# Performance work log

Measured on AMD Instinct MI355X. Metric: run time of the kernel, lower is better.

Reference implementation:

```python
import jax, jax.numpy as jnp
import numpy as np

EMBED_DIM = 1024
NUM_HEADS = 16
HEAD_DIM = EMBED_DIM // NUM_HEADS
FF_DIM = 4096
B, T = 4, 1024


def setup_inputs() -> dict:
    key = jax.random.key(0)
    ks = jax.random.split(key, 13)
    E, F = EMBED_DIM, FF_DIM
    s_e = 1.0 / np.sqrt(E)
    s_f = 1.0 / np.sqrt(F)
    return {
        "x": jax.random.normal(ks[0], (B, T, E), dtype=jnp.float32),
        "ln1_w": jnp.ones((E,), jnp.float32),
        "ln1_b": jnp.zeros((E,), jnp.float32),
        "ln2_w": jnp.ones((E,), jnp.float32),
        "ln2_b": jnp.zeros((E,), jnp.float32),
        "qkv_w": jax.random.uniform(ks[1], (3 * E, E), jnp.float32, -s_e, s_e),
        "qkv_b": jax.random.uniform(ks[2], (3 * E,), jnp.float32, -s_e, s_e),
        "out_w": jax.random.uniform(ks[3], (E, E), jnp.float32, -s_e, s_e),
        "out_b": jax.random.uniform(ks[4], (E,), jnp.float32, -s_e, s_e),
        "fc1_w": jax.random.uniform(ks[5], (F, E), jnp.float32, -s_e, s_e),
        "fc1_b": jax.random.uniform(ks[6], (F,), jnp.float32, -s_e, s_e),
        "fc2_w": jax.random.uniform(ks[7], (E, F), jnp.float32, -s_f, s_f),
        "fc2_b": jax.random.uniform(ks[8], (E,), jnp.float32, -s_f, s_f),
    }


def _layer_norm(x, w, b, eps=1e-5):
    mu = jnp.mean(x, axis=-1, keepdims=True)
    var = jnp.mean(jnp.square(x - mu), axis=-1, keepdims=True)
    return (x - mu) * jax.lax.rsqrt(var + eps) * w + b


def reference(x, ln1_w, ln1_b, ln2_w, ln2_b, qkv_w, qkv_b, out_w, out_b,
              fc1_w, fc1_b, fc2_w, fc2_b):
    Bn, Tn, C = x.shape
    H, D = NUM_HEADS, HEAD_DIM

    # --- causal self-attention (pre-LN) ---
    h = _layer_norm(x, ln1_w, ln1_b)
    qkv = h @ qkv_w.T + qkv_b  # [B,T,3E]
    qkv = qkv.reshape(Bn, Tn, 3, H, D).transpose(2, 0, 3, 1, 4)  # [3,B,H,T,D]
    q, k, v = qkv[0], qkv[1], qkv[2]
    scores = jnp.einsum("bhtd,bhsd->bhts", q, k) / np.sqrt(D).astype(np.float32)
    causal = jnp.tril(jnp.ones((Tn, Tn), dtype=bool))
    scores = jnp.where(causal, scores, -jnp.inf)
    probs = jax.nn.softmax(scores, axis=-1)  # dropout is identity at eval
    attn = jnp.einsum("bhts,bhsd->bhtd", probs, v)
    attn = attn.transpose(0, 2, 1, 3).reshape(Bn, Tn, C)
    attn = attn @ out_w.T + out_b
    x = x + attn

    # --- GELU MLP (pre-LN) ---
    h = _layer_norm(x, ln2_w, ln2_b)
    h = jax.nn.gelu(h @ fc1_w.T + fc1_b, approximate=False)
    h = h @ fc2_w.T + fc2_b
    return x + h
```

## Files before the change

### kernel.cpp

```cpp
#include <hip/hip_runtime.h>

typedef float floatx4 __attribute__((ext_vector_type(4)));
typedef short shortx8 __attribute__((ext_vector_type(8)));

#define E_DIM 1024
#define F_DIM 4096
#define BATCH 4
#define SEQ 1024
#define NH 16
#define HD 64
#define MROWS (BATCH*SEQ)
#define QKV_N (3*E_DIM)

typedef const __attribute__((address_space(1))) unsigned int* gas_ptr;
typedef __attribute__((address_space(3))) unsigned int* las_ptr;

__device__ __forceinline__ unsigned short f2bf(float f) {
    union { float f; unsigned u; } un; un.f = f;
    unsigned u = un.u;
    u += 0x7fffu + ((u >> 16) & 1u);
    return (unsigned short)(u >> 16);
}

__device__ __forceinline__ float gelu_fast(float v) {
    float u = 0.7978845608f * (v + 0.044715f * v * v * v);
    float t = __builtin_exp2f(-2.885390082f * u);
    return v * __builtin_amdgcn_rcpf(1.0f + t);
}

__device__ __forceinline__ void xcd_remap(int& m_idx, int& n_idx) {
    int nt = gridDim.x;
    int mt_x = gridDim.y >> 3;
    int lin = blockIdx.y * nt + blockIdx.x;
    int xcd = lin & 7, loc = lin >> 3;
    int n = loc / mt_x;
    int m_local = loc - n * mt_x;
    m_idx = xcd * mt_x + m_local;
    n_idx = n;
}

#define S_QKV (3*E_DIM*E_DIM)
#define S_WO  (E_DIM*E_DIM)
#define S_W1  (F_DIM*E_DIM)
#define S_TOT (S_QKV + S_WO + 2*S_W1)
__global__ __launch_bounds__(256) void f2b_all(
        const float* __restrict__ qkv_w, const float* __restrict__ out_w,
        const float* __restrict__ fc1_w, const float* __restrict__ fc2_w,
        unsigned short* __restrict__ wq, unsigned short* __restrict__ wo,
        unsigned short* __restrict__ w1, unsigned short* __restrict__ w2) {
    long idx = ((long)blockIdx.x * 256 + threadIdx.x) * 4;
    const float* src; unsigned short* dst; long off;
    if (idx < S_QKV)                    { src = qkv_w; dst = wq; off = idx; }
    else if (idx < S_QKV + S_WO)        { src = out_w; dst = wo; off = idx - S_QKV; }
    else if (idx < S_QKV + S_WO + S_W1) { src = fc1_w; dst = w1; off = idx - S_QKV - S_WO; }
    else                                { src = fc2_w; dst = w2; off = idx - S_QKV - S_WO - S_W1; }
    float4 v = *(const float4*)&src[off];
    ushort4 o;
    o.x = f2bf(v.x); o.y = f2bf(v.y); o.z = f2bf(v.z); o.w = f2bf(v.w);
    *(ushort4*)&dst[off] = o;
}

__global__ __launch_bounds__(256) void ln_kernel(const float* __restrict__ x,
                                                 const float* __restrict__ w,
                                                 const float* __restrict__ b,
                                                 unsigned short* __restrict__ out) {
    int row = blockIdx.x;
    const float* xr = x + (size_t)row * E_DIM;
    float v[4];
    float s = 0.f, ss = 0.f;
    for (int i = 0; i < 4; ++i) {
        v[i] = xr[threadIdx.x + i * 256];
        s += v[i]; ss += v[i] * v[i];
    }
    for (int m = 32; m; m >>= 1) { s += __shfl_xor(s, m); ss += __shfl_xor(ss, m); }
    __shared__ float red[8];
    int wave = threadIdx.x >> 6;
    if ((threadIdx.x & 63) == 0) { red[wave] = s; red[wave + 4] = ss; }
    __syncthreads();
    s = red[0] + red[1] + red[2] + red[3];
    ss = red[4] + red[5] + red[6] + red[7];
    float mu = s * (1.0f / E_DIM);
    float var = ss * (1.0f / E_DIM) - mu * mu;
    float rs = rsqrtf(var + 1e-5f);
    for (int i = 0; i < 4; ++i) {
        int c = threadIdx.x + i * 256;
        out[(size_t)row * E_DIM + c] = f2bf((v[i] - mu) * rs * w[c] + b[c]);
    }
}

#define TM 128
#define TN 128
#define BK 64

template<int EPI>
__global__ __launch_bounds__(256) void gemm_bt(
        const unsigned short* __restrict__ A, const unsigned short* __restrict__ Bw,
        const float* __restrict__ bias, const float* __restrict__ resid,
        float* __restrict__ Cf, unsigned short* __restrict__ Cb,
        int M, int N, int K) {
    __shared__ unsigned short sA[2][TM * BK];
    __shared__ unsigned short sB[2][TN * BK];
    int tid = threadIdx.x;
    int wave = tid >> 6, lane = tid & 63;
    int m_idx, n_idx;
    xcd_remap(m_idx, n_idx);
    int n0 = n_idx * TN, m0 = m_idx * TM;
    int wm = (wave & 1) * 64, wn = (wave >> 1) * 64;
    int l15 = lane & 15, quad = lane >> 4;

    int srow = wave * 32 + (lane >> 3);
    int scg  = (lane & 7) ^ (srow & 7);
    const unsigned short* Ag = A  + (size_t)(m0 + srow) * K + scg * 8;
    const unsigned short* Bg = Bw + (size_t)(n0 + srow) * K + scg * 8;

    floatx4 acc[4][4];
#pragma unroll
    for (int i = 0; i < 4; ++i)
#pragma unroll
        for (int j = 0; j < 4; ++j) acc[i][j] = (floatx4)0.f;

    auto stage = [&](int kt, int bsel) {
        int k0 = kt * BK;
#pragma unroll
        for (int p = 0; p < 4; ++p) {
            __builtin_amdgcn_global_load_lds((gas_ptr)(Ag + k0 + p * 8 * K),
                (las_ptr)&sA[bsel][(wave * 32 + p * 8) * BK], 16, 0, 0);
            __builtin_amdgcn_global_load_lds((gas_ptr)(Bg + k0 + p * 8 * K),
                (las_ptr)&sB[bsel][(wave * 32 + p * 8) * BK], 16, 0, 0);
        }
    };

    int T = K / BK;
    stage(0, 0);
    stage(1, 1);
    for (int i = 0; i < T; ++i) {
        if (i + 1 < T) { asm volatile("s_waitcnt vmcnt(8)" ::: "memory"); }
        else           { asm volatile("s_waitcnt vmcnt(0)" ::: "memory"); }
        __builtin_amdgcn_s_barrier();
        int bs = i & 1;
#pragma unroll
        for (int kk8 = 0; kk8 < 8; kk8 += 4) {
            shortx8 af[4], bfr[4];
#pragma unroll
            for (int ii = 0; ii < 4; ++ii) {
                int R = wm + ii * 16 + l15;
                int sc = (quad + kk8) ^ (R & 7);
                af[ii] = *(const shortx8*)&sA[bs][(R * 8 + sc) * 8];
            }
#pragma unroll
            for (int j = 0; j < 4; ++j) {
                int R = wn + j * 16 + l15;
                int sc = (quad + kk8) ^ (R & 7);
                bfr[j] = *(const shortx8*)&sB[bs][(R * 8 + sc) * 8];
            }
#pragma unroll
            for (int ii = 0; ii < 4; ++ii)
#pragma unroll
                for (int j = 0; j < 4; ++j)
                    acc[ii][j] = __builtin_amdgcn_mfma_f32_16x16x32_bf16(af[ii], bfr[j], acc[ii][j], 0, 0, 0);
        }
        __builtin_amdgcn_s_barrier();
        if (i + 2 < T) stage(i + 2, bs);
    }

#pragma unroll
    for (int i = 0; i < 4; ++i) {
        int row = m0 + wm + i * 16 + quad * 4;
#pragma unroll
        for (int j = 0; j < 4; ++j) {
            int col = n0 + wn + j * 16 + l15;
            float bs = bias[col];
#pragma unroll
            for (int r = 0; r < 4; ++r) {
                float v = acc[i][j][r] + bs;
                int rr = row + r;
                if (EPI & 1) v = gelu_fast(v);
                if (EPI & 2) v += resid[(size_t)rr * N + col];
                if (EPI & 4) Cf[(size_t)rr * N + col] = v;
                if (EPI & 8) Cb[(size_t)rr * N + col] = f2bf(v);
            }
        }
    }
}

template<int EPI>
__global__ __launch_bounds__(256) void gemm_n64(
        const unsigned short* __restrict__ A, const unsigned short* __restrict__ Bw,
        const float* __restrict__ bias, const float* __restrict__ resid,
        float* __restrict__ Cf, unsigned short* __restrict__ Cb,
        int M, int N, int K) {
    __shared__ unsigned short sA[3][TM * BK];
    __shared__ unsigned short sB[3][64 * BK];
    int tid = threadIdx.x;
    int wave = tid >> 6, lane = tid & 63;
    int m_idx, n_idx;
    xcd_remap(m_idx, n_idx);
    int n0 = n_idx * 64, m0 = m_idx * TM;
    int wm = (wave & 1) * 64, wn = (wave >> 1) * 32;
    int l15 = lane & 15, quad = lane >> 4;

    int srow = wave * 32 + (lane >> 3);
    int scg  = (lane & 7) ^ (srow & 7);
    const unsigned short* Ag = A + (size_t)(m0 + srow) * K + scg * 8;
    int srB  = wave * 16 + (lane >> 3);
    int scgB = (lane & 7) ^ (srB & 7);
    const unsigned short* Bg = Bw + (size_t)(n0 + srB) * K + scgB * 8;

    floatx4 acc[4][2];
#pragma unroll
    for (int i = 0; i < 4; ++i)
#pragma unroll
        for (int j = 0; j < 2; ++j) acc[i][j] = (floatx4)0.f;

    auto stage = [&](int kt, int bsel) {
        int k0 = kt * BK;
#pragma unroll
        for (int p = 0; p < 4; ++p)
            __builtin_amdgcn_global_load_lds((gas_ptr)(Ag + k0 + p * 8 * K),
                (las_ptr)&sA[bsel][(wave * 32 + p * 8) * BK], 16, 0, 0);
#pragma unroll
        for (int p = 0; p < 2; ++p)
            __builtin_amdgcn_global_load_lds((gas_ptr)(Bg + k0 + p * 8 * K),
                (las_ptr)&sB[bsel][(wave * 16 + p * 8) * BK], 16, 0, 0);
    };

    int T = K / BK;
    stage(0, 0);
    stage(1, 1);
    stage(2, 2);
    int bs = 0;
    for (int i = 0; i < T; ++i) {
        if (i + 2 < T)      { asm volatile("s_waitcnt vmcnt(12)" ::: "memory"); }
        else if (i + 1 < T) { asm volatile("s_waitcnt vmcnt(6)"  ::: "memory"); }
        else                { asm volatile("s_waitcnt vmcnt(0)"  ::: "memory"); }
        __builtin_amdgcn_s_barrier();
#pragma unroll
        for (int kk8 = 0; kk8 < 8; kk8 += 4) {
            shortx8 af[4], bfr[2];
#pragma unroll
            for (int ii = 0; ii < 4; ++ii) {
                int R = wm + ii * 16 + l15;
                int sc = (quad + kk8) ^ (R & 7);
                af[ii] = *(const shortx8*)&sA[bs][(R * 8 + sc) * 8];
            }
#pragma unroll
            for (int j = 0; j < 2; ++j) {
                int R = wn + j * 16 + l15;
                int sc = (quad + kk8) ^ (R & 7);
                bfr[j] = *(const shortx8*)&sB[bs][(R * 8 + sc) * 8];
            }
#pragma unroll
            for (int ii = 0; ii < 4; ++ii)
#pragma unroll
                for (int j = 0; j < 2; ++j)
                    acc[ii][j] = __builtin_amdgcn_mfma_f32_16x16x32_bf16(af[ii], bfr[j], acc[ii][j], 0, 0, 0);
        }
        __builtin_amdgcn_s_barrier();
        if (i + 3 < T) stage(i + 3, bs);
        bs = (bs == 2) ? 0 : bs + 1;
    }

#pragma unroll
    for (int i = 0; i < 4; ++i) {
        int row = m0 + wm + i * 16 + quad * 4;
#pragma unroll
        for (int j = 0; j < 2; ++j) {
            int col = n0 + wn + j * 16 + l15;
            float bs2 = bias[col];
#pragma unroll
            for (int r = 0; r < 4; ++r) {
                float v = acc[i][j][r] + bs2;
                int rr = row + r;
                if (EPI & 1) v = gelu_fast(v);
                if (EPI & 2) v += resid[(size_t)rr * N + col];
                if (EPI & 4) Cf[(size_t)rr * N + col] = v;
                if (EPI & 8) Cb[(size_t)rr * N + col] = f2bf(v);
            }
        }
    }
}

__global__ __launch_bounds__(256) void vtrans_kernel(const unsigned short* __restrict__ qkv,
                                                     unsigned short* __restrict__ vT) {
    __shared__ unsigned short tile[64 * 72];
    int tid = threadIdx.x;
    int bh = blockIdx.y, b = bh >> 4, h = bh & 15;
    int t0 = blockIdx.x * 64;
    const unsigned short* vsrc = qkv + (size_t)b * SEQ * QKV_N + 2 * E_DIM + h * HD;
#pragma unroll
    for (int p = 0; p < 2; ++p) {
        int idx = p * 256 + tid;
        int row = idx >> 3, col = (idx & 7) * 8;
        *(shortx8*)&tile[row * 72 + col] =
            *(const shortx8*)&vsrc[(size_t)(t0 + row) * QKV_N + col];
    }
    __syncthreads();
    int d = tid >> 2, tch = (tid & 3) * 16;
    unsigned short* dst = vT + (size_t)bh * HD * SEQ + (size_t)d * SEQ + t0 + tch;
    shortx8 a0, a1;
#pragma unroll
    for (int j = 0; j < 8; ++j) a0[j] = (short)tile[(tch + j) * 72 + d];
#pragma unroll
    for (int j = 0; j < 8; ++j) a1[j] = (short)tile[(tch + 8 + j) * 72 + d];
    *(shortx8*)&dst[0] = a0;
    *(shortx8*)&dst[8] = a1;
}

__global__ __launch_bounds__(256) void attn_kernel(
        const unsigned short* __restrict__ qkv, const unsigned short* __restrict__ vT,
        unsigned short* __restrict__ out) {
    __shared__ unsigned short kt[2][64 * 64];
    __shared__ unsigned short vt[2][64 * 64];
    __shared__ unsigned short ps[4][16 * 64];
    int tid = threadIdx.x;
    int wave = tid >> 6, lane = tid & 63, l15 = lane & 15, quad = lane >> 4;
    int bh = blockIdx.y, b = bh >> 4, h = bh & 15;
    const unsigned short* qbase = qkv + (size_t)b * SEQ * QKV_N + h * HD;
    const unsigned short* kbase = qbase + E_DIM;
    const unsigned short* vtb = vT + (size_t)bh * HD * SEQ;

    int srl = lane >> 3;
    int scg = (lane & 7) ^ srl;

    const float scale = 0.125f * 1.44269504f;

    auto stage = [&](int t, int bsel) {
        int s0 = t * 64;
#pragma unroll
        for (int p = 0; p < 2; ++p) {
            int rbase = p * 32 + wave * 8;
            __builtin_amdgcn_global_load_lds(
                (gas_ptr)&kbase[(size_t)(s0 + rbase + srl) * QKV_N + scg * 8],
                (las_ptr)&kt[bsel][rbase * 64], 16, 0, 0);
            __builtin_amdgcn_global_load_lds(
                (gas_ptr)&vtb[(size_t)(rbase + srl) * SEQ + s0 + scg * 8],
                (las_ptr)&vt[bsel][rbase * 64], 16, 0, 0);
        }
    };

    for (int pass = 0; pass < 2; ++pass) {
        int qt = (pass == 0) ? blockIdx.x : (15 - blockIdx.x);
        int q0 = qt * 64;
        int qrow = q0 + wave * 16;

        shortx8 qa0 = *(const shortx8*)&qbase[(size_t)(qrow + l15) * QKV_N + quad * 8];
        shortx8 qa1 = *(const shortx8*)&qbase[(size_t)(qrow + l15) * QKV_N + 32 + quad * 8];

        floatx4 o[4];
        for (int d = 0; d < 4; ++d) o[d] = (floatx4)0.f;
        float mrun[4], lrun[4];
        for (int r = 0; r < 4; ++r) { mrun[r] = -1e30f; lrun[r] = 0.f; }

        int ntile = qt + 1;
        __syncthreads();
        stage(0, 0);
        for (int t = 0; t < ntile; ++t) {
            asm volatile("s_waitcnt vmcnt(0)" ::: "memory");
            __builtin_amdgcn_s_barrier();
            if (t + 1 < ntile) stage(t + 1, (t + 1) & 1);
            int bsel = t & 1;
            int s0 = t * 64;

            floatx4 sfr[4];
#pragma unroll
            for (int ct = 0; ct < 4; ++ct) {
                int R = ct * 16 + l15;
                int sc0 = quad ^ (R & 7), sc1 = (4 + quad) ^ (R & 7);
                shortx8 kb0 = *(const shortx8*)&kt[bsel][(R * 8 + sc0) * 8];
                shortx8 kb1 = *(const shortx8*)&kt[bsel][(R * 8 + sc1) * 8];
                floatx4 s4 = (floatx4)0.f;
                s4 = __builtin_amdgcn_mfma_f32_16x16x32_bf16(qa0, kb0, s4, 0, 0, 0);
                s4 = __builtin_amdgcn_mfma_f32_16x16x32_bf16(qa1, kb1, s4, 0, 0, 0);
                sfr[ct] = s4;
            }

            bool masked = (t == ntile - 1);
#pragma unroll
            for (int r = 0; r < 4; ++r) {
                int qg = qrow + quad * 4 + r;
                float sv[4];
                float mx = mrun[r];
#pragma unroll
                for (int ct = 0; ct < 4; ++ct) {
                    float v = sfr[ct][r] * scale;
                    if (masked && (s0 + ct * 16 + l15 > qg)) v = -1e30f;
                    sv[ct] = v;
                    mx = fmaxf(mx, v);
                }
                for (int mm = 8; mm; mm >>= 1) mx = fmaxf(mx, __shfl_xor(mx, mm));
                float alpha = exp2f(mrun[r] - mx);
                mrun[r] = mx;
                float sum = 0.f;
                float pv[4];
#pragma unroll
                for (int ct = 0; ct < 4; ++ct) { pv[ct] = exp2f(sv[ct] - mx); sum += pv[ct]; }
                for (int mm = 8; mm; mm >>= 1) sum += __shfl_xor(sum, mm);
                lrun[r] = lrun[r] * alpha + sum;
#pragma unroll
                for (int d = 0; d < 4; ++d) o[d][r] *= alpha;
                int row = quad * 4 + r;
#pragma unroll
                for (int ct = 0; ct < 4; ++ct) {
                    int g = ct * 2 + (l15 >> 3);
                    int sc = g ^ (row & 7);
                    ps[wave][row * 64 + sc * 8 + (l15 & 7)] = f2bf(pv[ct]);
                }
            }
            shortx8 pa0, pa1;
            {
                int sc0 = quad ^ (l15 & 7), sc1 = (4 + quad) ^ (l15 & 7);
                pa0 = *(const shortx8*)&ps[wave][(l15 * 8 + sc0) * 8];
                pa1 = *(const shortx8*)&ps[wave][(l15 * 8 + sc1) * 8];
            }
#pragma unroll
            for (int d = 0; d < 4; ++d) {
                int R = d * 16 + l15;
                int sc0 = quad ^ (R & 7), sc1 = (4 + quad) ^ (R & 7);
                shortx8 vb0 = *(const shortx8*)&vt[bsel][(R * 8 + sc0) * 8];
                shortx8 vb1 = *(const shortx8*)&vt[bsel][(R * 8 + sc1) * 8];
                o[d] = __builtin_amdgcn_mfma_f32_16x16x32_bf16(pa0, vb0, o[d], 0, 0, 0);
                o[d] = __builtin_amdgcn_mfma_f32_16x16x32_bf16(pa1, vb1, o[d], 0, 0, 0);
            }
        }

#pragma unroll
        for (int r = 0; r < 4; ++r) {
            float inv = 1.0f / lrun[r];
            int m = (b << 10) + qrow + quad * 4 + r;
#pragma unroll
            for (int d = 0; d < 4; ++d)
                out[(size_t)m * E_DIM + h * HD + d * 16 + l15] = f2bf(o[d][r] * inv);
        }
    }
}

extern "C" void kernel_launch(void* const* d_in, const int* in_sizes, int n_in,
                              void* d_out, int out_size, void* d_ws, size_t ws_size,
                              hipStream_t stream) {
    const float* x     = (const float*)d_in[0];
    const float* ln1_w = (const float*)d_in[1];
    const float* ln1_b = (const float*)d_in[2];
    const float* ln2_w = (const float*)d_in[3];
    const float* ln2_b = (const float*)d_in[4];
    const float* qkv_w = (const float*)d_in[5];
    const float* qkv_b = (const float*)d_in[6];
    const float* out_w = (const float*)d_in[7];
    const float* out_b = (const float*)d_in[8];
    const float* fc1_w = (const float*)d_in[9];
    const float* fc1_b = (const float*)d_in[10];
    const float* fc2_w = (const float*)d_in[11];
    const float* fc2_b = (const float*)d_in[12];

    char* ws = (char*)d_ws;
    size_t off = 0;
    auto alloc = [&](size_t bytes) { char* p = ws + off; off += bytes; return p; };
    unsigned short* wq   = (unsigned short*)alloc((size_t)3 * E_DIM * E_DIM * 2);
    unsigned short* wo   = (unsigned short*)alloc((size_t)E_DIM * E_DIM * 2);
    unsigned short* w1   = (unsigned short*)alloc((size_t)F_DIM * E_DIM * 2);
    unsigned short* w2   = (unsigned short*)alloc((size_t)E_DIM * F_DIM * 2);
    unsigned short* h1   = (unsigned short*)alloc((size_t)MROWS * E_DIM * 2);
    unsigned short* qkvb = (unsigned short*)alloc((size_t)MROWS * QKV_N * 2);
    unsigned short* vT   = (unsigned short*)alloc((size_t)BATCH * NH * HD * SEQ * 2);
    unsigned short* attn = (unsigned short*)alloc((size_t)MROWS * E_DIM * 2);
    float*          x1   = (float*)alloc((size_t)MROWS * E_DIM * 4);
    unsigned short* h2   = (unsigned short*)alloc((size_t)MROWS * E_DIM * 2);
    unsigned short* g    = (unsigned short*)alloc((size_t)MROWS * F_DIM * 2);

    f2b_all<<<S_TOT / 4 / 256, 256, 0, stream>>>(qkv_w, out_w, fc1_w, fc2_w, wq, wo, w1, w2);

    ln_kernel<<<MROWS, 256, 0, stream>>>(x, ln1_w, ln1_b, h1);
    gemm_bt<8><<<dim3(QKV_N / TN, MROWS / TM), 256, 0, stream>>>(
        h1, wq, qkv_b, nullptr, nullptr, qkvb, MROWS, QKV_N, E_DIM);
    vtrans_kernel<<<dim3(SEQ / 64, BATCH * NH), 256, 0, stream>>>(qkvb, vT);
    attn_kernel<<<dim3(8, BATCH * NH), 256, 0, stream>>>(qkvb, vT, attn);
    gemm_n64<2 | 4><<<dim3(E_DIM / 64, MROWS / TM), 256, 0, stream>>>(
        attn, wo, out_b, x, x1, nullptr, MROWS, E_DIM, E_DIM);
    ln_kernel<<<MROWS, 256, 0, stream>>>(x1, ln2_w, ln2_b, h2);
    gemm_bt<1 | 8><<<dim3(F_DIM / TN, MROWS / TM), 256, 0, stream>>>(
        h2, w1, fc1_b, nullptr, nullptr, g, MROWS, F_DIM, E_DIM);
    gemm_n64<2 | 4><<<dim3(E_DIM / 64, MROWS / TM), 256, 0, stream>>>(
        g, w2, fc2_b, x1, (float*)d_out, nullptr, MROWS, E_DIM, F_DIM);
}
```

Measured before the change: 330.1 us.

## Add 256x256-tile 512-thread GEMM kernel for QKV and FC1 projections

Adds a new GEMM kernel that computes a 256x256 output tile per block with 8 waves, double-buffered LDS staging through global_load_lds, and raised wave priority around the MFMA bursts. The QKV and FC1 GEMMs now use it in place of the older gemm_bt tiles. Larger tiles raise arithmetic intensity and cut global and L2 traffic per FLOP. The cost is fewer blocks, which can hurt load balance (QKV gets 192 blocks), plus higher register and LDS pressure and only two stages of buffering.

New measurement: 332.2 us. Within noise of the previous version (+0.6%).

```diff
diff --git a/kernel.cpp b/kernel.cpp
--- a/kernel.cpp
+++ b/kernel.cpp
@@ -184,6 +184,103 @@
 }
 
 template<int EPI>
+__global__ __launch_bounds__(512, 2) void gemm_256(
+        const unsigned short* __restrict__ A, const unsigned short* __restrict__ Bw,
+        const float* __restrict__ bias, const float* __restrict__ resid,
+        float* __restrict__ Cf, unsigned short* __restrict__ Cb,
+        int M, int N, int K) {
+    __shared__ unsigned short sA[2][256 * BK];
+    __shared__ unsigned short sB[2][256 * BK];
+    int tid = threadIdx.x;
+    int wave = tid >> 6, lane = tid & 63;
+    int m_idx, n_idx;
+    xcd_remap(m_idx, n_idx);
+    int m0 = m_idx * 256, n0 = n_idx * 256;
+    int wm = (wave >> 2) * 128, wn = (wave & 3) * 64;
+    int l15 = lane & 15, quad = lane >> 4;
+
+    int srow = tid >> 3;
+    int scg  = (tid & 7) ^ (srow & 7);
+    const unsigned short* Ag = A  + (size_t)(m0 + srow) * K + scg * 8;
+    const unsigned short* Bg = Bw + (size_t)(n0 + srow) * K + scg * 8;
+
+    floatx4 acc[8][4];
+#pragma unroll
+    for (int i = 0; i < 8; ++i)
+#pragma unroll
+        for (int j = 0; j < 4; ++j) acc[i][j] = (floatx4)0.f;
+
+    auto stage = [&](int kt, int bsel) {
+        int k0 = kt * BK;
+#pragma unroll
+        for (int r = 0; r < 4; ++r)
+            __builtin_amdgcn_global_load_lds((gas_ptr)(Ag + k0 + (size_t)r * 64 * K),
+                (las_ptr)&sA[bsel][(r * 64 + wave * 8) * BK], 16, 0, 0);
+#pragma unroll
+        for (int r = 0; r < 4; ++r)
+            __builtin_amdgcn_global_load_lds((gas_ptr)(Bg + k0 + (size_t)r * 64 * K),
+                (las_ptr)&sB[bsel][(r * 64 + wave * 8) * BK], 16, 0, 0);
+    };
+
+    int T = K / BK;
+    stage(0, 0);
+    for (int i = 0; i < T; ++i) {
+        asm volatile("s_waitcnt vmcnt(0)" ::: "memory");
+        __builtin_amdgcn_s_barrier();
+        int bs = i & 1;
+        if (i + 1 < T) stage(i + 1, bs ^ 1);
+#pragma unroll
+        for (int ks = 0; ks < 2; ++ks) {
+            int kk8 = ks * 4;
+            shortx8 bfr[4];
+#pragma unroll
+            for (int j = 0; j < 4; ++j) {
+                int R = wn + j * 16 + l15;
+                int sc = (quad + kk8) ^ (R & 7);
+                bfr[j] = *(const shortx8*)&sB[bs][(R * 8 + sc) * 8];
+            }
+#pragma unroll
+            for (int mh = 0; mh < 2; ++mh) {
+                shortx8 af[4];
+#pragma unroll
+                for (int ii = 0; ii < 4; ++ii) {
+                    int R = wm + mh * 64 + ii * 16 + l15;
+                    int sc = (quad + kk8) ^ (R & 7);
+                    af[ii] = *(const shortx8*)&sA[bs][(R * 8 + sc) * 8];
+                }
+                __builtin_amdgcn_s_setprio(1);
+#pragma unroll
+                for (int ii = 0; ii < 4; ++ii)
+#pragma unroll
+                    for (int j = 0; j < 4; ++j)
+                        acc[mh * 4 + ii][j] = __builtin_amdgcn_mfma_f32_16x16x32_bf16(
+                            af[ii], bfr[j], acc[mh * 4 + ii][j], 0, 0, 0);
+                __builtin_amdgcn_s_setprio(0);
+            }
+        }
+    }
+
+#pragma unroll
+    for (int i = 0; i < 8; ++i) {
+        int row = m0 + wm + i * 16 + quad * 4;
+#pragma unroll
+        for (int j = 0; j < 4; ++j) {
+            int col = n0 + wn + j * 16 + l15;
+            float bs2 = bias[col];
+#pragma unroll
+            for (int r = 0; r < 4; ++r) {
+                float v = acc[i][j][r] + bs2;
+                int rr = row + r;
+                if (EPI & 1) v = gelu_fast(v);
+                if (EPI & 2) v += resid[(size_t)rr * N + col];
+                if (EPI & 4) Cf[(size_t)rr * N + col] = v;
+                if (EPI & 8) Cb[(size_t)rr * N + col] = f2bf(v);
+            }
+        }
+    }
+}
+
+template<int EPI>
 __global__ __launch_bounds__(256) void gemm_n64(
         const unsigned short* __restrict__ A, const unsigned short* __restrict__ Bw,
         const float* __restrict__ bias, const float* __restrict__ resid,
@@ -469,14 +566,14 @@
     f2b_all<<<S_TOT / 4 / 256, 256, 0, stream>>>(qkv_w, out_w, fc1_w, fc2_w, wq, wo, w1, w2);
 
     ln_kernel<<<MROWS, 256, 0, stream>>>(x, ln1_w, ln1_b, h1);
-    gemm_bt<8><<<dim3(QKV_N / TN, MROWS / TM), 256, 0, stream>>>(
+    gemm_256<8><<<dim3(QKV_N / 256, MROWS / 256), 512, 0, stream>>>(
         h1, wq, qkv_b, nullptr, nullptr, qkvb, MROWS, QKV_N, E_DIM);
     vtrans_kernel<<<dim3(SEQ / 64, BATCH * NH), 256, 0, stream>>>(qkvb, vT);
     attn_kernel<<<dim3(8, BATCH * NH), 256, 0, stream>>>(qkvb, vT, attn);
     gemm_n64<2 | 4><<<dim3(E_DIM / 64, MROWS / TM), 256, 0, stream>>>(
         attn, wo, out_b, x, x1, nullptr, MROWS, E_DIM, E_DIM);
     ln_kernel<<<MROWS, 256, 0, stream>>>(x1, ln2_w, ln2_b, h2);
-    gemm_bt<1 | 8><<<dim3(F_DIM / TN, MROWS / TM), 256, 0, stream>>>(
+    gemm_256<1 | 8><<<dim3(F_DIM / 256, MROWS / 256), 512, 0, stream>>>(
         h2, w1, fc1_b, nullptr, nullptr, g, MROWS, F_DIM, E_DIM);
     gemm_n64<2 | 4><<<dim3(E_DIM / 64, MROWS / TM), 256, 0, stream>>>(
         g, w2, fc2_b, x1, (float*)d_out, nullptr, MROWS, E_DIM, F_DIM);
```

## Replace 128x128 GEMM with 256x256 eight-wave tile and interleaved prefetch schedule

Applied to the files above, without the earlier changes.

The QKV and FC1 GEMMs now use a 256x256 output tile computed by 512 threads (8 waves). Each wave owns 32 rows across all 256 columns. Loads for the next k-step are split into four chunks and issued between the four MFMA sub-phases, with s_setprio raising priority around the MFMA bursts. The larger tile raises arithmetic intensity and operand reuse from LDS and global memory. In exchange it needs 64 KiB of LDS and a high register count for 32 accumulators per wave, and the grid shrinks to 192 and 256 blocks, which may underfill the GPU.

Result: no change. 326.4 us (-1.1%).

```diff
diff --git a/kernel.cpp b/kernel.cpp
--- a/kernel.cpp
+++ b/kernel.cpp
@@ -93,86 +93,110 @@
 #define BK 64
 
 template<int EPI>
-__global__ __launch_bounds__(256) void gemm_bt(
+__global__ __launch_bounds__(512, 2) void gemm_8p(
         const unsigned short* __restrict__ A, const unsigned short* __restrict__ Bw,
         const float* __restrict__ bias, const float* __restrict__ resid,
         float* __restrict__ Cf, unsigned short* __restrict__ Cb,
         int M, int N, int K) {
-    __shared__ unsigned short sA[2][TM * BK];
-    __shared__ unsigned short sB[2][TN * BK];
+    __shared__ unsigned short sA[2][2][128 * 64];
+    __shared__ unsigned short sB[2][2][128 * 64];
     int tid = threadIdx.x;
     int wave = tid >> 6, lane = tid & 63;
-    int m_idx, n_idx;
-    xcd_remap(m_idx, n_idx);
-    int n0 = n_idx * TN, m0 = m_idx * TM;
-    int wm = (wave & 1) * 64, wn = (wave >> 1) * 64;
+    int m_idx, n_idx; xcd_remap(m_idx, n_idx);
+    int m0 = m_idx * 256, n0 = n_idx * 256;
+    int ha = wave >> 2;
+    int wa = (wave & 3) * 32;
     int l15 = lane & 15, quad = lane >> 4;
 
-    int srow = wave * 32 + (lane >> 3);
-    int scg  = (lane & 7) ^ (srow & 7);
-    const unsigned short* Ag = A  + (size_t)(m0 + srow) * K + scg * 8;
-    const unsigned short* Bg = Bw + (size_t)(n0 + srow) * K + scg * 8;
-
-    floatx4 acc[4][4];
-#pragma unroll
-    for (int i = 0; i < 4; ++i)
-#pragma unroll
-        for (int j = 0; j < 4; ++j) acc[i][j] = (floatx4)0.f;
-
-    auto stage = [&](int kt, int bsel) {
-        int k0 = kt * BK;
-#pragma unroll
-        for (int p = 0; p < 4; ++p) {
-            __builtin_amdgcn_global_load_lds((gas_ptr)(Ag + k0 + p * 8 * K),
-                (las_ptr)&sA[bsel][(wave * 32 + p * 8) * BK], 16, 0, 0);
-            __builtin_amdgcn_global_load_lds((gas_ptr)(Bg + k0 + p * 8 * K),
-                (las_ptr)&sB[bsel][(wave * 32 + p * 8) * BK], 16, 0, 0);
-        }
+    int rowlane = lane >> 3;
+    int scg = (lane & 7) ^ rowlane;
+    const unsigned short* PA = A  + (size_t)(m0 + wave * 16 + rowlane) * K + scg * 8;
+    const unsigned short* PB = Bw + (size_t)(n0 + wave * 16 + rowlane) * K + scg * 8;
+
+    floatx4 acc[2][16];
+#pragma unroll
+    for (int i = 0; i < 2; ++i)
+#pragma unroll
+        for (int j = 0; j < 16; ++j) acc[i][j] = (floatx4)0.f;
+
+    auto stageA = [&](int kt, int h, int b) {
+#pragma unroll
+        for (int p = 0; p < 2; ++p)
+            __builtin_amdgcn_global_load_lds(
+                (gas_ptr)(PA + (size_t)(h * 128 + p * 8) * K + kt * 64),
+                (las_ptr)&sA[b][h][(wave * 16 + p * 8) * 64], 16, 0, 0);
     };
+    auto stageB = [&](int kt, int h, int b) {
+#pragma unroll
+        for (int p = 0; p < 2; ++p)
+            __builtin_amdgcn_global_load_lds(
+                (gas_ptr)(PB + (size_t)(h * 128 + p * 8) * K + kt * 64),
+                (las_ptr)&sB[b][h][(wave * 16 + p * 8) * 64], 16, 0, 0);
+    };
 
     int T = K / BK;
-    stage(0, 0);
-    stage(1, 1);
-    for (int i = 0; i < T; ++i) {
-        if (i + 1 < T) { asm volatile("s_waitcnt vmcnt(8)" ::: "memory"); }
-        else           { asm volatile("s_waitcnt vmcnt(0)" ::: "memory"); }
+    stageA(0, 0, 0); stageA(0, 1, 0); stageB(0, 0, 0); stageB(0, 1, 0);
+
+    for (int t = 0; t < T; ++t) {
+        int b = t & 1, nb = b ^ 1;
+        bool hn = (t + 1 < T);
+        asm volatile("s_waitcnt vmcnt(2)" ::: "memory");
         __builtin_amdgcn_s_barrier();
-        int bs = i & 1;
-#pragma unroll
-        for (int kk8 = 0; kk8 < 8; kk8 += 4) {
-            shortx8 af[4], bfr[4];
-#pragma unroll
-            for (int ii = 0; ii < 4; ++ii) {
-                int R = wm + ii * 16 + l15;
-                int sc = (quad + kk8) ^ (R & 7);
-                af[ii] = *(const shortx8*)&sA[bs][(R * 8 + sc) * 8];
-            }
-#pragma unroll
-            for (int j = 0; j < 4; ++j) {
-                int R = wn + j * 16 + l15;
-                int sc = (quad + kk8) ^ (R & 7);
-                bfr[j] = *(const shortx8*)&sB[bs][(R * 8 + sc) * 8];
-            }
-#pragma unroll
-            for (int ii = 0; ii < 4; ++ii)
-#pragma unroll
-                for (int j = 0; j < 4; ++j)
-                    acc[ii][j] = __builtin_amdgcn_mfma_f32_16x16x32_bf16(af[ii], bfr[j], acc[ii][j], 0, 0, 0);
-        }
-        __builtin_amdgcn_s_barrier();
-        if (i + 2 < T) stage(i + 2, bs);
-    }
-
-#pragma unroll
-    for (int i = 0; i < 4; ++i) {
-        int row = m0 + wm + i * 16 + quad * 4;
-#pragma unroll
-        for (int j = 0; j < 4; ++j) {
-            int col = n0 + wn + j * 16 + l15;
-            float bs = bias[col];
+        shortx8 af[2][2];
+#pragma unroll
+        for (int ii = 0; ii < 2; ++ii)
+#pragma unroll
+            for (int ks = 0; ks < 2; ++ks) {
+                int ra = wa + ii * 16 + l15;
+                int g = (quad + ks * 4) ^ (ra & 7);
+                af[ii][ks] = *(const shortx8*)&sA[b][ha][(ra * 8 + g) * 8];
+            }
+#pragma unroll
+        for (int q = 0; q < 4; ++q) {
+            shortx8 bfr[4][2];
+#pragma unroll
+            for (int j = 0; j < 4; ++j)
+#pragma unroll
+                for (int ks = 0; ks < 2; ++ks) {
+                    int rb = (q & 1) * 64 + j * 16 + l15;
+                    int g = (quad + ks * 4) ^ (rb & 7);
+                    bfr[j][ks] = *(const shortx8*)&sB[b][q >> 1][(rb * 8 + g) * 8];
+                }
+            if (hn) {
+                if (q == 0)      stageA(t + 1, 0, nb);
+                else if (q == 1) stageA(t + 1, 1, nb);
+                else if (q == 2) stageB(t + 1, 0, nb);
+                else             stageB(t + 1, 1, nb);
+            }
+            __builtin_amdgcn_s_barrier();
+            __builtin_amdgcn_s_setprio(1);
+#pragma unroll
+            for (int ks = 0; ks < 2; ++ks)
+#pragma unroll
+                for (int ii = 0; ii < 2; ++ii)
+#pragma unroll
+                    for (int j = 0; j < 4; ++j)
+                        acc[ii][q * 4 + j] = __builtin_amdgcn_mfma_f32_16x16x32_bf16(
+                            af[ii][ks], bfr[j][ks], acc[ii][q * 4 + j], 0, 0, 0);
+            __builtin_amdgcn_s_setprio(0);
+            if (q == 1) {
+                if (hn) asm volatile("s_waitcnt vmcnt(4)" ::: "memory");
+                else    asm volatile("s_waitcnt vmcnt(0)" ::: "memory");
+            }
+            if (q < 3) __builtin_amdgcn_s_barrier();
+        }
+    }
+
+#pragma unroll
+    for (int ii = 0; ii < 2; ++ii) {
+        int row = m0 + wave * 32 + ii * 16 + quad * 4;
+#pragma unroll
+        for (int ci = 0; ci < 16; ++ci) {
+            int col = n0 + ci * 16 + l15;
+            float bs2 = bias[col];
 #pragma unroll
             for (int r = 0; r < 4; ++r) {
-                float v = acc[i][j][r] + bs;
+                float v = acc[ii][ci][r] + bs2;
                 int rr = row + r;
                 if (EPI & 1) v = gelu_fast(v);
                 if (EPI & 2) v += resid[(size_t)rr * N + col];
@@ -469,14 +493,14 @@
     f2b_all<<<S_TOT / 4 / 256, 256, 0, stream>>>(qkv_w, out_w, fc1_w, fc2_w, wq, wo, w1, w2);
 
     ln_kernel<<<MROWS, 256, 0, stream>>>(x, ln1_w, ln1_b, h1);
-    gemm_bt<8><<<dim3(QKV_N / TN, MROWS / TM), 256, 0, stream>>>(
+    gemm_8p<8><<<dim3(QKV_N / 256, MROWS / 256), 512, 0, stream>>>(
         h1, wq, qkv_b, nullptr, nullptr, qkvb, MROWS, QKV_N, E_DIM);
     vtrans_kernel<<<dim3(SEQ / 64, BATCH * NH), 256, 0, stream>>>(qkvb, vT);
     attn_kernel<<<dim3(8, BATCH * NH), 256, 0, stream>>>(qkvb, vT, attn);
     gemm_n64<2 | 4><<<dim3(E_DIM / 64, MROWS / TM), 256, 0, stream>>>(
         attn, wo, out_b, x, x1, nullptr, MROWS, E_DIM, E_DIM);
     ln_kernel<<<MROWS, 256, 0, stream>>>(x1, ln2_w, ln2_b, h2);
-    gemm_bt<1 | 8><<<dim3(F_DIM / TN, MROWS / TM), 256, 0, stream>>>(
+    gemm_8p<1 | 8><<<dim3(F_DIM / 256, MROWS / 256), 512, 0, stream>>>(
         h2, w1, fc1_b, nullptr, nullptr, g, MROWS, F_DIM, E_DIM);
     gemm_n64<2 | 4><<<dim3(E_DIM / 64, MROWS / TM), 256, 0, stream>>>(
         g, w2, fc2_b, x1, (float*)d_out, nullptr, MROWS, E_DIM, F_DIM);
```

## Use 256x256 tiles with 16 waves for wide GEMMs and 8 waves for N64 GEMMs

Applied to the files above, without the earlier changes.

Replaces the 128x128, 4-wave GEMM used for the QKV and FC1 projections with a 256x256 tile kernel run by 1024 threads (16 waves, 64x64 each). The larger tile raises operand reuse per LDS load. The N=64 GEMM moves from 4 waves with triple buffering to 8 waves with 32x32 per-wave tiles and double buffering. Risks include fewer workgroups per grid (wave quantization on 256 CUs), 128KB of LDS per block in the large kernel, and a shallower prefetch pipeline in the N64 kernel.

After: 315.2 us. 4.5% less time.

```diff
diff --git a/kernel.cpp b/kernel.cpp
--- a/kernel.cpp
+++ b/kernel.cpp
@@ -93,152 +93,145 @@
 #define BK 64
 
 template<int EPI>
-__global__ __launch_bounds__(256) void gemm_bt(
+__global__ __launch_bounds__(1024) void gemm_16w(
+        const unsigned short* __restrict__ A, const unsigned short* __restrict__ Bw,
+        const float* __restrict__ bias, const float* __restrict__ resid,
+        float* __restrict__ Cf, unsigned short* __restrict__ Cb,
+        int M, int N, int K) {
+    __shared__ unsigned short sA[2][256 * BK];
+    __shared__ unsigned short sB[2][256 * BK];
+    int tid = threadIdx.x;
+    int wave = tid >> 6, lane = tid & 63;
+    int m_idx, n_idx; xcd_remap(m_idx, n_idx);
+    int m0 = m_idx * 256, n0 = n_idx * 256;
+    int wm = (wave >> 2) * 64, wn = (wave & 3) * 64;
+    int l15 = lane & 15, quad = lane >> 4;
+
+    int srow = tid >> 3;
+    int scg  = (tid & 7) ^ (srow & 7);
+    const unsigned short* Ag = A  + (size_t)(m0 + srow) * K + scg * 8;
+    const unsigned short* Bg = Bw + (size_t)(n0 + srow) * K + scg * 8;
+
+    floatx4 acc[4][4];
+#pragma unroll
+    for (int i = 0; i < 4; ++i)
+#pragma unroll
+        for (int j = 0; j < 4; ++j) acc[i][j] = (floatx4)0.f;
+
+    auto stage = [&](int kt, int bsel) {
+        int k0 = kt * BK;
+#pragma unroll
+        for (int p = 0; p < 2; ++p) {
+            __builtin_amdgcn_global_load_lds((gas_ptr)(Ag + k0 + (size_t)p * 128 * K),
+                (las_ptr)&sA[bsel][(p * 128 + wave * 8) * BK], 16, 0, 0);
+            __builtin_amdgcn_global_load_lds((gas_ptr)(Bg + k0 + (size_t)p * 128 * K),
+                (las_ptr)&sB[bsel][(p * 128 + wave * 8) * BK], 16, 0, 0);
+        }
+    };
+
+    int T = K / BK;
+    stage(0, 0);
+    stage(1, 1);
+    for (int i = 0; i < T; ++i) {
+        if (i + 1 < T) { asm volatile("s_waitcnt vmcnt(4)" ::: "memory"); }
+        else           { asm volatile("s_waitcnt vmcnt(0)" ::: "memory"); }
+        __builtin_amdgcn_s_barrier();
+        int bs = i & 1;
+#pragma unroll
+        for (int kk8 = 0; kk8 < 8; kk8 += 4) {
+            shortx8 af[4], bfr[4];
+#pragma unroll
+            for (int ii = 0; ii < 4; ++ii) {
+                int R = wm + ii * 16 + l15;
+                int sc = (quad + kk8) ^ (R & 7);
+                af[ii] = *(const shortx8*)&sA[bs][(R * 8 + sc) * 8];
+            }
+#pragma unroll
+            for (int j = 0; j < 4; ++j) {
+                int R = wn + j * 16 + l15;
+                int sc = (quad + kk8) ^ (R & 7);
+                bfr[j] = *(const shortx8*)&sB[bs][(R * 8 + sc) * 8];
+            }
+#pragma unroll
+            for (int ii = 0; ii < 4; ++ii)
+#pragma unroll
+                for (int j = 0; j < 4; ++j)
+                    acc[ii][j] = __builtin_amdgcn_mfma_f32_16x16x32_bf16(af[ii], bfr[j], acc[ii][j], 0, 0, 0);
+        }
+        __builtin_amdgcn_s_barrier();
+        if (i + 2 < T) stage(i + 2, bs);
+    }
+
+#pragma unroll
+    for (int i = 0; i < 4; ++i) {
+        int row = m0 + wm + i * 16 + quad * 4;
+#pragma unroll
+        for (int j = 0; j < 4; ++j) {
+            int col = n0 + wn + j * 16 + l15;
+            float bs2 = bias[col];
+#pragma unroll
+            for (int r = 0; r < 4; ++r) {
+                float v = acc[i][j][r] + bs2;
+                int rr = row + r;
+                if (EPI & 1) v = gelu_fast(v);
+                if (EPI & 2) v += resid[(size_t)rr * N + col];
+                if (EPI & 4) Cf[(size_t)rr * N + col] = v;
+                if (EPI & 8) Cb[(size_t)rr * N + col] = f2bf(v);
+            }
+        }
+    }
+}
+
+template<int EPI>
+__global__ __launch_bounds__(512) void gemm_n64(
         const unsigned short* __restrict__ A, const unsigned short* __restrict__ Bw,
         const float* __restrict__ bias, const float* __restrict__ resid,
         float* __restrict__ Cf, unsigned short* __restrict__ Cb,
         int M, int N, int K) {
     __shared__ unsigned short sA[2][TM * BK];
-    __shared__ unsigned short sB[2][TN * BK];
-    int tid = threadIdx.x;
-    int wave = tid >> 6, lane = tid & 63;
-    int m_idx, n_idx;
-    xcd_remap(m_idx, n_idx);
-    int n0 = n_idx * TN, m0 = m_idx * TM;
-    int wm = (wave & 1) * 64, wn = (wave >> 1) * 64;
-    int l15 = lane & 15, quad = lane >> 4;
-
-    int srow = wave * 32 + (lane >> 3);
-    int scg  = (lane & 7) ^ (srow & 7);
-    const unsigned short* Ag = A  + (size_t)(m0 + srow) * K + scg * 8;
-    const unsigned short* Bg = Bw + (size_t)(n0 + srow) * K + scg * 8;
-
-    floatx4 acc[4][4];
-#pragma unroll
-    for (int i = 0; i < 4; ++i)
-#pragma unroll
-        for (int j = 0; j < 4; ++j) acc[i][j] = (floatx4)0.f;
-
-    auto stage = [&](int kt, int bsel) {
-        int k0 = kt * BK;
-#pragma unroll
-        for (int p = 0; p < 4; ++p) {
-            __builtin_amdgcn_global_load_lds((gas_ptr)(Ag + k0 + p * 8 * K),
-                (las_ptr)&sA[bsel][(wave * 32 + p * 8) * BK], 16, 0, 0);
-            __builtin_amdgcn_global_load_lds((gas_ptr)(Bg + k0 + p * 8 * K),
-                (las_ptr)&sB[bsel][(wave * 32 + p * 8) * BK], 16, 0, 0);
-        }
-    };
-
-    int T = K / BK;
-    stage(0, 0);
-    stage(1, 1);
-    for (int i = 0; i < T; ++i) {
-        if (i + 1 < T) { asm volatile("s_waitcnt vmcnt(8)" ::: "memory"); }
-        else           { asm volatile("s_waitcnt vmcnt(0)" ::: "memory"); }
-        __builtin_amdgcn_s_barrier();
-        int bs = i & 1;
-#pragma unroll
-        for (int kk8 = 0; kk8 < 8; kk8 += 4) {
-            shortx8 af[4], bfr[4];
-#pragma unroll
-            for (int ii = 0; ii < 4; ++ii) {
-                int R = wm + ii * 16 + l15;
-                int sc = (quad + kk8) ^ (R & 7);
-                af[ii] = *(const shortx8*)&sA[bs][(R * 8 + sc) * 8];
-            }
-#pragma unroll
-            for (int j = 0; j < 4; ++j) {
-                int R = wn + j * 16 + l15;
-                int sc = (quad + kk8) ^ (R & 7);
-                bfr[j] = *(const shortx8*)&sB[bs][(R * 8 + sc) * 8];
-            }
-#pragma unroll
-            for (int ii = 0; ii < 4; ++ii)
-#pragma unroll
-                for (int j = 0; j < 4; ++j)
-                    acc[ii][j] = __builtin_amdgcn_mfma_f32_16x16x32_bf16(af[ii], bfr[j], acc[ii][j], 0, 0, 0);
-        }
-        __builtin_amdgcn_s_barrier();
-        if (i + 2 < T) stage(i + 2, bs);
-    }
-
-#pragma unroll
-    for (int i = 0; i < 4; ++i) {
-        int row = m0 + wm + i * 16 + quad * 4;
-#pragma unroll
-        for (int j = 0; j < 4; ++j) {
-            int col = n0 + wn + j * 16 + l15;
-            float bs = bias[col];
-#pragma unroll
-            for (int r = 0; r < 4; ++r) {
-                float v = acc[i][j][r] + bs;
-                int rr = row + r;
-                if (EPI & 1) v = gelu_fast(v);
-                if (EPI & 2) v += resid[(size_t)rr * N + col];
-                if (EPI & 4) Cf[(size_t)rr * N + col] = v;
-                if (EPI & 8) Cb[(size_t)rr * N + col] = f2bf(v);
-            }
-        }
-    }
-}
-
-template<int EPI>
-__global__ __launch_bounds__(256) void gemm_n64(
-        const unsigned short* __restrict__ A, const unsigned short* __restrict__ Bw,
-        const float* __restrict__ bias, const float* __restrict__ resid,
-        float* __restrict__ Cf, unsigned short* __restrict__ Cb,
-        int M, int N, int K) {
-    __shared__ unsigned short sA[3][TM * BK];
-    __shared__ unsigned short sB[3][64 * BK];
+    __shared__ unsigned short sB[2][64 * BK];
     int tid = threadIdx.x;
     int wave = tid >> 6, lane = tid & 63;
     int m_idx, n_idx;
     xcd_remap(m_idx, n_idx);
     int n0 = n_idx * 64, m0 = m_idx * TM;
-    int wm = (wave & 1) * 64, wn = (wave >> 1) * 32;
+    int wm = (wave & 3) * 32, wn = (wave >> 2) * 32;
     int l15 = lane & 15, quad = lane >> 4;
 
-    int srow = wave * 32 + (lane >> 3);
+    int srow = wave * 8 + (lane >> 3);
     int scg  = (lane & 7) ^ (srow & 7);
-    const unsigned short* Ag = A + (size_t)(m0 + srow) * K + scg * 8;
-    int srB  = wave * 16 + (lane >> 3);
-    int scgB = (lane & 7) ^ (srB & 7);
-    const unsigned short* Bg = Bw + (size_t)(n0 + srB) * K + scgB * 8;
-
-    floatx4 acc[4][2];
-#pragma unroll
-    for (int i = 0; i < 4; ++i)
+    const unsigned short* Ag = A  + (size_t)(m0 + srow) * K + scg * 8;
+    const unsigned short* Bg = Bw + (size_t)(n0 + srow) * K + scg * 8;
+
+    floatx4 acc[2][2];
+#pragma unroll
+    for (int i = 0; i < 2; ++i)
 #pragma unroll
         for (int j = 0; j < 2; ++j) acc[i][j] = (floatx4)0.f;
 
     auto stage = [&](int kt, int bsel) {
         int k0 = kt * BK;
 #pragma unroll
-        for (int p = 0; p < 4; ++p)
-            __builtin_amdgcn_global_load_lds((gas_ptr)(Ag + k0 + p * 8 * K),
-                (las_ptr)&sA[bsel][(wave * 32 + p * 8) * BK], 16, 0, 0);
-#pragma unroll
         for (int p = 0; p < 2; ++p)
-            __builtin_amdgcn_global_load_lds((gas_ptr)(Bg + k0 + p * 8 * K),
-                (las_ptr)&sB[bsel][(wave * 16 + p * 8) * BK], 16, 0, 0);
+            __builtin_amdgcn_global_load_lds((gas_ptr)(Ag + k0 + (size_t)p * 64 * K),
+                (las_ptr)&sA[bsel][(p * 64 + wave * 8) * BK], 16, 0, 0);
+        __builtin_amdgcn_global_load_lds((gas_ptr)(Bg + k0),
+            (las_ptr)&sB[bsel][(wave * 8) * BK], 16, 0, 0);
     };
 
     int T = K / BK;
     stage(0, 0);
     stage(1, 1);
-    stage(2, 2);
-    int bs = 0;
     for (int i = 0; i < T; ++i) {
-        if (i + 2 < T)      { asm volatile("s_waitcnt vmcnt(12)" ::: "memory"); }
-        else if (i + 1 < T) { asm volatile("s_waitcnt vmcnt(6)"  ::: "memory"); }
-        else                { asm volatile("s_waitcnt vmcnt(0)"  ::: "memory"); }
+        if (i + 1 < T) { asm volatile("s_waitcnt vmcnt(3)" ::: "memory"); }
+        else           { asm volatile("s_waitcnt vmcnt(0)" ::: "memory"); }
         __builtin_amdgcn_s_barrier();
+        int bs = i & 1;
 #pragma unroll
         for (int kk8 = 0; kk8 < 8; kk8 += 4) {
-            shortx8 af[4], bfr[2];
-#pragma unroll
-            for (int ii = 0; ii < 4; ++ii) {
+            shortx8 af[2], bfr[2];
+#pragma unroll
+            for (int ii = 0; ii < 2; ++ii) {
                 int R = wm + ii * 16 + l15;
                 int sc = (quad + kk8) ^ (R & 7);
                 af[ii] = *(const shortx8*)&sA[bs][(R * 8 + sc) * 8];
@@ -250,18 +243,17 @@
                 bfr[j] = *(const shortx8*)&sB[bs][(R * 8 + sc) * 8];
             }
 #pragma unroll
-            for (int ii = 0; ii < 4; ++ii)
+            for (int ii = 0; ii < 2; ++ii)
 #pragma unroll
                 for (int j = 0; j < 2; ++j)
                     acc[ii][j] = __builtin_amdgcn_mfma_f32_16x16x32_bf16(af[ii], bfr[j], acc[ii][j], 0, 0, 0);
         }
         __builtin_amdgcn_s_barrier();
-        if (i + 3 < T) stage(i + 3, bs);
-        bs = (bs == 2) ? 0 : bs + 1;
-    }
-
-#pragma unroll
-    for (int i = 0; i < 4; ++i) {
+        if (i + 2 < T) stage(i + 2, bs);
+    }
+
+#pragma unroll
+    for (int i = 0; i < 2; ++i) {
         int row = m0 + wm + i * 16 + quad * 4;
 #pragma unroll
         for (int j = 0; j < 2; ++j) {
@@ -469,15 +461,15 @@
     f2b_all<<<S_TOT / 4 / 256, 256, 0, stream>>>(qkv_w, out_w, fc1_w, fc2_w, wq, wo, w1, w2);
 
     ln_kernel<<<MROWS, 256, 0, stream>>>(x, ln1_w, ln1_b, h1);
-    gemm_bt<8><<<dim3(QKV_N / TN, MROWS / TM), 256, 0, stream>>>(
+    gemm_16w<8><<<dim3(QKV_N / 256, MROWS / 256), 1024, 0, stream>>>(
         h1, wq, qkv_b, nullptr, nullptr, qkvb, MROWS, QKV_N, E_DIM);
     vtrans_kernel<<<dim3(SEQ / 64, BATCH * NH), 256, 0, stream>>>(qkvb, vT);
     attn_kernel<<<dim3(8, BATCH * NH), 256, 0, stream>>>(qkvb, vT, attn);
-    gemm_n64<2 | 4><<<dim3(E_DIM / 64, MROWS / TM), 256, 0, stream>>>(
+    gemm_n64<2 | 4><<<dim3(E_DIM / 64, MROWS / TM), 512, 0, stream>>>(
         attn, wo, out_b, x, x1, nullptr, MROWS, E_DIM, E_DIM);
     ln_kernel<<<MROWS, 256, 0, stream>>>(x1, ln2_w, ln2_b, h2);
-    gemm_bt<1 | 8><<<dim3(F_DIM / TN, MROWS / TM), 256, 0, stream>>>(
+    gemm_16w<1 | 8><<<dim3(F_DIM / 256, MROWS / 256), 1024, 0, stream>>>(
         h2, w1, fc1_b, nullptr, nullptr, g, MROWS, F_DIM, E_DIM);
-    gemm_n64<2 | 4><<<dim3(E_DIM / 64, MROWS / TM), 256, 0, stream>>>(
+    gemm_n64<2 | 4><<<dim3(E_DIM / 64, MROWS / TM), 512, 0, stream>>>(
         g, w2, fc2_b, x1, (float*)d_out, nullptr, MROWS, E_DIM, F_DIM);
 }
```
